# Kernel optimization log

Measured on AMD Instinct MI355X. Metric: run time of the kernel, lower is better.

The kernel has to match this reference:

```python
import jax, jax.numpy as jnp
import numpy as np

EPS = 1e-3  # keras LayerNormalization default epsilon

def layer_norm(x, gamma, beta):
    mu = jnp.mean(x, axis=-1, keepdims=True)
    var = jnp.var(x, axis=-1, keepdims=True)
    return (x - mu) * jax.lax.rsqrt(var + EPS) * gamma + beta

def setup_inputs() -> dict:
    key = jax.random.key(0)
    ks = jax.random.split(key, 10)
    B, N, FD, AD, PD, DP = 4, 512, 256, 256, 128, 64
    s = lambda k, *sh: jax.random.normal(k, sh, dtype=jnp.float32)
    return {
        "F": s(ks[0], B, N, FD),
        "D": s(ks[1], B, N, N, DP),
        "Wq": s(ks[2], FD, AD) / np.sqrt(FD),
        "Wk": s(ks[3], FD, AD) / np.sqrt(FD),
        "Wv": s(ks[4], FD, AD) / np.sqrt(FD),
        "g_f": jnp.ones((FD,), jnp.float32),
        "b_f": jnp.zeros((FD,), jnp.float32),
        "g_p": jnp.ones((DP,), jnp.float32),
        "b_p": jnp.zeros((DP,), jnp.float32),
        "W_pt": s(ks[5], DP, PD) / np.sqrt(DP),
        "b_pt": jnp.zeros((PD,), jnp.float32),
        "W_ph": s(ks[6], PD, 1) / np.sqrt(PD),
    }

def reference(F, D, Wq, Wk, Wv, g_f, b_f, g_p, b_p, W_pt, b_pt, W_ph):
    # features path
    Fn = layer_norm(F, g_f, b_f)                       # [B,N,FD]
    Q = Fn @ Wq                                        # [B,N,AD]
    K = Fn @ Wk
    V = Fn @ Wv
    # pair-bias path: LN -> Dense(pairs_dim)+bias -> Dense(num_heads=1)
    Bn = layer_norm(D, g_p, b_p)                       # [B,N,N,DP]
    Bt = Bn @ W_pt + b_pt                              # [B,N,N,PD]
    bias = (Bt @ W_ph)[..., 0]                         # [B,N,N]
    scalar = 1.0 / jnp.sqrt(jnp.float32(Q.shape[-1]))
    A = jnp.einsum('bqd,bkd->bqk', Q, K) + bias        # QK^T + pair bias
    A = jax.nn.softmax(scalar * A, axis=-1)
    O = jnp.einsum('bqk,bkd->bqd', A, V)               # [B,N,AD]
    return jnp.sum(O, axis=-1)                         # [B,N]
```

## Files before the change

### kernel.cpp

```cpp
#include <hip/hip_runtime.h>
#include <cstddef>
#include <cstdint>

#define OFF_GW    0
#define OFF_WV    64
#define OFF_SC    320
#define OFF_VSUM  384
#define OFF_Q     2432
#define OFF_K     526720

typedef float v4f __attribute__((ext_vector_type(4)));

__global__ __launch_bounds__(256) void k0_consts(
    const float* __restrict__ Wv, const float* __restrict__ g_p,
    const float* __restrict__ b_p, const float* __restrict__ W_pt,
    const float* __restrict__ b_pt, const float* __restrict__ W_ph,
    float* __restrict__ ws) {
  int t = threadIdx.x;
  if (blockIdx.x < 64) {
    int row = blockIdx.x * 4 + (t >> 6);
    int l = t & 63;
    float s = 0.f;
#pragma unroll
    for (int j = 0; j < 4; ++j) s += Wv[row * 256 + l + 64 * j];
    for (int m = 32; m >= 1; m >>= 1) s += __shfl_xor(s, m);
    if (l == 0) ws[OFF_WV + row] = s;
  } else {
    __shared__ float wc_s[64];
    __shared__ float wph_s[128];
    if (t < 128) wph_s[t] = W_ph[t];
    __syncthreads();
    int c = t >> 2, sub = t & 3;
    float wc = 0.f;
#pragma unroll
    for (int j = 0; j < 32; ++j)
      wc += W_pt[c * 128 + sub * 32 + j] * wph_s[sub * 32 + j];
    wc += __shfl_xor(wc, 1);
    wc += __shfl_xor(wc, 2);
    if (sub == 0) {
      wc_s[c] = wc;
      ws[OFF_GW + c] = g_p[c] * wc;
    }
    __syncthreads();
    if (t == 0) {
      float sg = 0.f, bc = 0.f;
      for (int cc = 0; cc < 64; ++cc) {
        sg += g_p[cc] * wc_s[cc];
        bc += b_p[cc] * wc_s[cc];
      }
      for (int p = 0; p < 128; ++p) bc += b_pt[p] * wph_s[p];
      ws[OFF_SC] = sg;
      ws[OFF_SC + 1] = bc;
    }
  }
}

__global__ __launch_bounds__(256) void k1_ln_qk(
    const float* __restrict__ F, const float* __restrict__ Wq,
    const float* __restrict__ Wk, const float* __restrict__ g_f,
    const float* __restrict__ b_f, float* __restrict__ ws) {
  __shared__ __align__(16) float fn[8][260];
  __shared__ float smu[8], srn[8];
  int t = threadIdx.x;
  int g = blockIdx.x >> 1, h = blockIdx.x & 1;
  int row0 = g * 8;
  const float* Fp = F + (size_t)row0 * 256;
#pragma unroll
  for (int k = 0; k < 8; ++k) fn[k][t] = Fp[k * 256 + t];
  __syncthreads();
  int r = t >> 5, l32 = t & 31;
  float s1 = 0.f, s2 = 0.f;
#pragma unroll
  for (int m = 0; m < 8; ++m) {
    float x = fn[r][l32 + 32 * m];
    s1 += x;
    s2 += x * x;
  }
  for (int m = 16; m >= 1; m >>= 1) {
    s1 += __shfl_xor(s1, m);
    s2 += __shfl_xor(s2, m);
  }
  if (l32 == 0) {
    float mu = s1 * (1.f / 256.f);
    float var = s2 * (1.f / 256.f) - mu * mu;
    smu[r] = mu;
    srn[r] = rsqrtf(var + 1e-3f);
  }
  __syncthreads();
  float gf = g_f[t], bf = b_f[t];
#pragma unroll
  for (int k = 0; k < 8; ++k)
    fn[k][t] = (fn[k][t] - smu[k]) * srn[k] * gf + bf;
  __syncthreads();
  if (h == 0) {
    const float* wv = ws + OFF_WV;
    float s = 0.f;
#pragma unroll
    for (int m = 0; m < 8; ++m) s += fn[r][l32 + 32 * m] * wv[l32 + 32 * m];
    for (int m = 16; m >= 1; m >>= 1) s += __shfl_xor(s, m);
    if (l32 == 0) ws[OFF_VSUM + row0 + r] = s;
  }
  int matsel = t >> 7;
  int col = h * 128 + (t & 127);
  const float* W = matsel ? Wk : Wq;
  float acc[8] = {0, 0, 0, 0, 0, 0, 0, 0};
#pragma unroll 2
  for (int f = 0; f < 256; f += 4) {
    float w0 = W[(f + 0) * 256 + col];
    float w1 = W[(f + 1) * 256 + col];
    float w2 = W[(f + 2) * 256 + col];
    float w3 = W[(f + 3) * 256 + col];
#pragma unroll
    for (int k = 0; k < 8; ++k) {
      v4f x = *(const v4f*)(&fn[k][f]);
      acc[k] = fmaf(x.w, w3,
               fmaf(x.z, w2, fmaf(x.y, w1, fmaf(x.x, w0, acc[k]))));
    }
  }
  float* Out = ws + (matsel ? OFF_K : OFF_Q) + (size_t)row0 * 256 + col;
#pragma unroll
  for (int k = 0; k < 8; ++k) Out[k * 256] = acc[k];
}

__global__ __launch_bounds__(256) void kb_bias_attn(
    const float* __restrict__ D, const float* __restrict__ ws,
    float* __restrict__ out) {
  __shared__ float Sx[4][512];
  __shared__ __align__(16) float Qs[4][256];
  __shared__ float vs[512];
  int t = threadIdx.x;
  int w = t >> 6, l = t & 63;
  int b = blockIdx.x >> 7, tile = blockIdx.x & 127;
  int rowbase = b * 512 + tile * 4;

#pragma unroll
  for (int k = 0; k < 4; ++k)
    Qs[k][t] = ws[OFF_Q + (size_t)(rowbase + k) * 256 + t];
  vs[t] = ws[OFF_VSUM + b * 512 + t];
  vs[t + 256] = ws[OFF_VSUM + b * 512 + 256 + t];
  float sum_gw = ws[OFF_SC];
  float bconst = ws[OFF_SC + 1];
  v4f g[16];
#pragma unroll
  for (int p = 0; p < 16; ++p) g[p] = *(const v4f*)(ws + OFF_GW + p * 4);

  const float* Dw = D + (size_t)(rowbase + w) * (512 * 64);
#pragma unroll 1
  for (int i = 0; i < 8; ++i) {
    const v4f* e = (const v4f*)(Dw + (size_t)(i * 64 + l) * 64);
    v4f x[16];
#pragma unroll
    for (int p = 0; p < 16; ++p) x[p] = e[p];
    float s1 = 0.f, s2 = 0.f, sw = 0.f;
#pragma unroll
    for (int p = 0; p < 16; ++p) {
      v4f xx = x[p];
      s1 += xx.x + xx.y + xx.z + xx.w;
      s2 += xx.x * xx.x + xx.y * xx.y + xx.z * xx.z + xx.w * xx.w;
      sw += xx.x * g[p].x + xx.y * g[p].y + xx.z * g[p].z + xx.w * g[p].w;
    }
    float mu = s1 * (1.f / 64.f);
    float var = s2 * (1.f / 64.f) - mu * mu;
    float rn = rsqrtf(var + 1e-3f);
    Sx[w][i * 64 + l] = (rn * (sw - mu * sum_gw) + bconst) * 0.0625f;
  }
  __syncthreads();

  const float* Kg = ws + OFF_K;
  const v4f* K0p = (const v4f*)(Kg + (size_t)(b * 512 + t) * 256);
  const v4f* K1p = (const v4f*)(Kg + (size_t)(b * 512 + 256 + t) * 256);
  float a0[4] = {0, 0, 0, 0}, a1[4] = {0, 0, 0, 0};
#pragma unroll 8
  for (int f = 0; f < 64; ++f) {
    v4f kv0 = K0p[f];
    v4f kv1 = K1p[f];
#pragma unroll
    for (int rr = 0; rr < 4; ++rr) {
      v4f qv = *(const v4f*)(&Qs[rr][f * 4]);
      a0[rr] += qv.x * kv0.x + qv.y * kv0.y + qv.z * kv0.z + qv.w * kv0.w;
      a1[rr] += qv.x * kv1.x + qv.y * kv1.y + qv.z * kv1.z + qv.w * kv1.w;
    }
  }
#pragma unroll
  for (int rr = 0; rr < 4; ++rr) {
    Sx[rr][t] += a0[rr] * 0.0625f;
    Sx[rr][t + 256] += a1[rr] * 0.0625f;
  }
  __syncthreads();

  float m = -1e30f;
#pragma unroll
  for (int j = 0; j < 8; ++j) m = fmaxf(m, Sx[w][l + 64 * j]);
  for (int mm = 32; mm >= 1; mm >>= 1) m = fmaxf(m, __shfl_xor(m, mm));
  float se = 0.f, sv = 0.f;
#pragma unroll
  for (int j = 0; j < 8; ++j) {
    float ev = __expf(Sx[w][l + 64 * j] - m);
    se += ev;
    sv += ev * vs[l + 64 * j];
  }
  for (int mm = 32; mm >= 1; mm >>= 1) {
    se += __shfl_xor(se, mm);
    sv += __shfl_xor(sv, mm);
  }
  if (l == 0) out[rowbase + w] = sv / se;
}

extern "C" void kernel_launch(void* const* d_in, const int* in_sizes, int n_in,
                              void* d_out, int out_size, void* d_ws,
                              size_t ws_size, hipStream_t stream) {
  const float* F    = (const float*)d_in[0];
  const float* D    = (const float*)d_in[1];
  const float* Wq   = (const float*)d_in[2];
  const float* Wk   = (const float*)d_in[3];
  const float* Wv   = (const float*)d_in[4];
  const float* g_f  = (const float*)d_in[5];
  const float* b_f  = (const float*)d_in[6];
  const float* g_p  = (const float*)d_in[7];
  const float* b_p  = (const float*)d_in[8];
  const float* W_pt = (const float*)d_in[9];
  const float* b_pt = (const float*)d_in[10];
  const float* W_ph = (const float*)d_in[11];
  float* out = (float*)d_out;
  float* ws = (float*)d_ws;

  k0_consts<<<65, 256, 0, stream>>>(Wv, g_p, b_p, W_pt, b_pt, W_ph, ws);
  k1_ln_qk<<<512, 256, 0, stream>>>(F, Wq, Wk, g_f, b_f, ws);
  kb_bias_attn<<<512, 256, 0, stream>>>(D, ws, out);
}
```

Before: 443.1 us.

## Transpose K in workspace and coalesce D loads with 16-lane row reductions

K is now written transposed per batch, [col][row], so the attention kernel reads contiguous float2 pairs across threads instead of strided rows of K. Reading D changes from one thread per 64-float row to 16 lanes cooperating on each row with v4f loads, followed by shuffle reductions. Both changes target uncoalesced global memory access in the bandwidth-bound pair-bias stage. In exchange there are many more shuffle instructions, and the transposed K stores in k1 are scattered writes.

```diff
diff --git a/kernel.cpp b/kernel.cpp
--- a/kernel.cpp
+++ b/kernel.cpp
@@ -7,9 +7,10 @@
 #define OFF_SC    320
 #define OFF_VSUM  384
 #define OFF_Q     2432
-#define OFF_K     526720
+#define OFF_KT    526720
 
 typedef float v4f __attribute__((ext_vector_type(4)));
+typedef float v2f __attribute__((ext_vector_type(2)));
 
 __global__ __launch_bounds__(256) void k0_consts(
     const float* __restrict__ Wv, const float* __restrict__ g_p,
@@ -117,9 +118,18 @@
                fmaf(x.z, w2, fmaf(x.y, w1, fmaf(x.x, w0, acc[k]))));
     }
   }
-  float* Out = ws + (matsel ? OFF_K : OFF_Q) + (size_t)row0 * 256 + col;
-#pragma unroll
-  for (int k = 0; k < 8; ++k) Out[k * 256] = acc[k];
+  if (matsel == 0) {
+    float* Out = ws + OFF_Q + (size_t)row0 * 256 + col;
+#pragma unroll
+    for (int k = 0; k < 8; ++k) Out[k * 256] = acc[k];
+  } else {
+    int bb = row0 >> 9, r0b = row0 & 511;
+    float* Out = ws + OFF_KT + (size_t)bb * 131072 + (size_t)col * 512 + r0b;
+    v4f o0 = {acc[0], acc[1], acc[2], acc[3]};
+    v4f o1 = {acc[4], acc[5], acc[6], acc[7]};
+    *(v4f*)Out = o0;
+    *(v4f*)(Out + 4) = o1;
+  }
 }
 
 __global__ __launch_bounds__(256) void kb_bias_attn(
@@ -140,51 +150,52 @@
   vs[t + 256] = ws[OFF_VSUM + b * 512 + 256 + t];
   float sum_gw = ws[OFF_SC];
   float bconst = ws[OFF_SC + 1];
-  v4f g[16];
-#pragma unroll
-  for (int p = 0; p < 16; ++p) g[p] = *(const v4f*)(ws + OFF_GW + p * 4);
-
+
+  int l16 = l & 15, lg = l >> 4;
+  v4f gv = *(const v4f*)(ws + OFF_GW + l16 * 4);
   const float* Dw = D + (size_t)(rowbase + w) * (512 * 64);
-#pragma unroll 1
-  for (int i = 0; i < 8; ++i) {
-    const v4f* e = (const v4f*)(Dw + (size_t)(i * 64 + l) * 64);
-    v4f x[16];
-#pragma unroll
-    for (int p = 0; p < 16; ++p) x[p] = e[p];
-    float s1 = 0.f, s2 = 0.f, sw = 0.f;
-#pragma unroll
-    for (int p = 0; p < 16; ++p) {
-      v4f xx = x[p];
-      s1 += xx.x + xx.y + xx.z + xx.w;
-      s2 += xx.x * xx.x + xx.y * xx.y + xx.z * xx.z + xx.w * xx.w;
-      sw += xx.x * g[p].x + xx.y * g[p].y + xx.z * g[p].z + xx.w * g[p].w;
-    }
-    float mu = s1 * (1.f / 64.f);
-    float var = s2 * (1.f / 64.f) - mu * mu;
-    float rn = rsqrtf(var + 1e-3f);
-    Sx[w][i * 64 + l] = (rn * (sw - mu * sum_gw) + bconst) * 0.0625f;
-  }
-  __syncthreads();
-
-  const float* Kg = ws + OFF_K;
-  const v4f* K0p = (const v4f*)(Kg + (size_t)(b * 512 + t) * 256);
-  const v4f* K1p = (const v4f*)(Kg + (size_t)(b * 512 + 256 + t) * 256);
+#pragma unroll 8
+  for (int i = 0; i < 128; ++i) {
+    v4f x = *(const v4f*)(Dw + (size_t)(4 * i + lg) * 64 + l16 * 4);
+    float s1 = x.x + x.y + x.z + x.w;
+    float s2 = x.x * x.x + x.y * x.y + x.z * x.z + x.w * x.w;
+    float sw = x.x * gv.x + x.y * gv.y + x.z * gv.z + x.w * gv.w;
+#pragma unroll
+    for (int m = 1; m <= 8; m <<= 1) {
+      s1 += __shfl_xor(s1, m);
+      s2 += __shfl_xor(s2, m);
+      sw += __shfl_xor(sw, m);
+    }
+    if (l16 == 0) {
+      float mu = s1 * (1.f / 64.f);
+      float var = s2 * (1.f / 64.f) - mu * mu;
+      float rn = rsqrtf(var + 1e-3f);
+      Sx[w][4 * i + lg] = (rn * (sw - mu * sum_gw) + bconst) * 0.0625f;
+    }
+  }
+  __syncthreads();
+
+  const float* Ktb = ws + OFF_KT + (size_t)b * 131072;
   float a0[4] = {0, 0, 0, 0}, a1[4] = {0, 0, 0, 0};
-#pragma unroll 8
-  for (int f = 0; f < 64; ++f) {
-    v4f kv0 = K0p[f];
-    v4f kv1 = K1p[f];
-#pragma unroll
-    for (int rr = 0; rr < 4; ++rr) {
-      v4f qv = *(const v4f*)(&Qs[rr][f * 4]);
-      a0[rr] += qv.x * kv0.x + qv.y * kv0.y + qv.z * kv0.z + qv.w * kv0.w;
-      a1[rr] += qv.x * kv1.x + qv.y * kv1.y + qv.z * kv1.z + qv.w * kv1.w;
+#pragma unroll 2
+  for (int f4 = 0; f4 < 64; ++f4) {
+    v4f qv0 = *(const v4f*)(&Qs[0][f4 * 4]);
+    v4f qv1 = *(const v4f*)(&Qs[1][f4 * 4]);
+    v4f qv2 = *(const v4f*)(&Qs[2][f4 * 4]);
+    v4f qv3 = *(const v4f*)(&Qs[3][f4 * 4]);
+#pragma unroll
+    for (int ff = 0; ff < 4; ++ff) {
+      v2f kv = *(const v2f*)(Ktb + (size_t)(f4 * 4 + ff) * 512 + 2 * t);
+      a0[0] += qv0[ff] * kv.x; a1[0] += qv0[ff] * kv.y;
+      a0[1] += qv1[ff] * kv.x; a1[1] += qv1[ff] * kv.y;
+      a0[2] += qv2[ff] * kv.x; a1[2] += qv2[ff] * kv.y;
+      a0[3] += qv3[ff] * kv.x; a1[3] += qv3[ff] * kv.y;
     }
   }
 #pragma unroll
   for (int rr = 0; rr < 4; ++rr) {
-    Sx[rr][t] += a0[rr] * 0.0625f;
-    Sx[rr][t + 256] += a1[rr] * 0.0625f;
+    Sx[rr][2 * t]     += a0[rr] * 0.0625f;
+    Sx[rr][2 * t + 1] += a1[rr] * 0.0625f;
   }
   __syncthreads();
 
```

After: 454.8 us. +2.7%, slower.

## Split bias-attention into 2-row blocks of 512 threads for more parallelism

Applied to the files above, without the earlier changes.

Restructures the main bias-attention kernel so each 512-thread block handles two query rows instead of four. Eight waves share the per-pair LayerNorm work on D, and the gamma*w vector moves from registers into shared memory. This launches more blocks and waves to hide memory latency while streaming D. In exchange, each K tile is reused by fewer query rows, so K is read from cache twice as often, and half the waves idle during the softmax.

```diff
diff --git a/kernel.cpp b/kernel.cpp
--- a/kernel.cpp
+++ b/kernel.cpp
@@ -122,88 +122,85 @@
   for (int k = 0; k < 8; ++k) Out[k * 256] = acc[k];
 }
 
-__global__ __launch_bounds__(256) void kb_bias_attn(
+__global__ __launch_bounds__(512, 4) void kb_bias_attn(
     const float* __restrict__ D, const float* __restrict__ ws,
     float* __restrict__ out) {
-  __shared__ float Sx[4][512];
-  __shared__ __align__(16) float Qs[4][256];
+  __shared__ float Sx[2][512];
+  __shared__ __align__(16) float Qs[2][256];
   __shared__ float vs[512];
+  __shared__ __align__(16) float gws[64];
   int t = threadIdx.x;
   int w = t >> 6, l = t & 63;
-  int b = blockIdx.x >> 7, tile = blockIdx.x & 127;
-  int rowbase = b * 512 + tile * 4;
-
-#pragma unroll
-  for (int k = 0; k < 4; ++k)
-    Qs[k][t] = ws[OFF_Q + (size_t)(rowbase + k) * 256 + t];
+  int b = blockIdx.x >> 8, pair = blockIdx.x & 255;
+  int rowbase = b * 512 + pair * 2;
+
+  if (t < 256) Qs[0][t] = ws[OFF_Q + (size_t)rowbase * 256 + t];
+  else         Qs[1][t - 256] = ws[OFF_Q + (size_t)(rowbase + 1) * 256 + (t - 256)];
   vs[t] = ws[OFF_VSUM + b * 512 + t];
-  vs[t + 256] = ws[OFF_VSUM + b * 512 + 256 + t];
+  if (t < 64) gws[t] = ws[OFF_GW + t];
   float sum_gw = ws[OFF_SC];
   float bconst = ws[OFF_SC + 1];
-  v4f g[16];
-#pragma unroll
-  for (int p = 0; p < 16; ++p) g[p] = *(const v4f*)(ws + OFF_GW + p * 4);
-
-  const float* Dw = D + (size_t)(rowbase + w) * (512 * 64);
+  __syncthreads();
+
+  {
+    int row = w >> 2, quar = w & 3;
+    const float* Dw = D + (size_t)(rowbase + row) * (512 * 64);
 #pragma unroll 1
-  for (int i = 0; i < 8; ++i) {
-    const v4f* e = (const v4f*)(Dw + (size_t)(i * 64 + l) * 64);
-    v4f x[16];
-#pragma unroll
-    for (int p = 0; p < 16; ++p) x[p] = e[p];
-    float s1 = 0.f, s2 = 0.f, sw = 0.f;
-#pragma unroll
-    for (int p = 0; p < 16; ++p) {
-      v4f xx = x[p];
-      s1 += xx.x + xx.y + xx.z + xx.w;
-      s2 += xx.x * xx.x + xx.y * xx.y + xx.z * xx.z + xx.w * xx.w;
-      sw += xx.x * g[p].x + xx.y * g[p].y + xx.z * g[p].z + xx.w * g[p].w;
-    }
-    float mu = s1 * (1.f / 64.f);
-    float var = s2 * (1.f / 64.f) - mu * mu;
-    float rn = rsqrtf(var + 1e-3f);
-    Sx[w][i * 64 + l] = (rn * (sw - mu * sum_gw) + bconst) * 0.0625f;
-  }
-  __syncthreads();
-
-  const float* Kg = ws + OFF_K;
-  const v4f* K0p = (const v4f*)(Kg + (size_t)(b * 512 + t) * 256);
-  const v4f* K1p = (const v4f*)(Kg + (size_t)(b * 512 + 256 + t) * 256);
-  float a0[4] = {0, 0, 0, 0}, a1[4] = {0, 0, 0, 0};
+    for (int i = 0; i < 2; ++i) {
+      int e = quar * 128 + i * 64 + l;
+      const v4f* ep = (const v4f*)(Dw + (size_t)e * 64);
+      v4f x[16];
+#pragma unroll
+      for (int p = 0; p < 16; ++p) x[p] = ep[p];
+      float s1 = 0.f, s2 = 0.f, sw = 0.f;
+#pragma unroll
+      for (int p = 0; p < 16; ++p) {
+        v4f xx = x[p];
+        v4f gv = *(const v4f*)(&gws[p * 4]);
+        s1 += xx.x + xx.y + xx.z + xx.w;
+        s2 += xx.x * xx.x + xx.y * xx.y + xx.z * xx.z + xx.w * xx.w;
+        sw += xx.x * gv.x + xx.y * gv.y + xx.z * gv.z + xx.w * gv.w;
+      }
+      float mu = s1 * (1.f / 64.f);
+      float var = s2 * (1.f / 64.f) - mu * mu;
+      float rn = rsqrtf(var + 1e-3f);
+      Sx[row][e] = (rn * (sw - mu * sum_gw) + bconst) * 0.0625f;
+    }
+  }
+  __syncthreads();
+
+  const float* Kp = ws + OFF_K + (size_t)(b * 512 + t) * 256;
+  float a0 = 0.f, a1 = 0.f;
 #pragma unroll 8
-  for (int f = 0; f < 64; ++f) {
-    v4f kv0 = K0p[f];
-    v4f kv1 = K1p[f];
-#pragma unroll
-    for (int rr = 0; rr < 4; ++rr) {
-      v4f qv = *(const v4f*)(&Qs[rr][f * 4]);
-      a0[rr] += qv.x * kv0.x + qv.y * kv0.y + qv.z * kv0.z + qv.w * kv0.w;
-      a1[rr] += qv.x * kv1.x + qv.y * kv1.y + qv.z * kv1.z + qv.w * kv1.w;
-    }
-  }
-#pragma unroll
-  for (int rr = 0; rr < 4; ++rr) {
-    Sx[rr][t] += a0[rr] * 0.0625f;
-    Sx[rr][t + 256] += a1[rr] * 0.0625f;
-  }
-  __syncthreads();
-
-  float m = -1e30f;
-#pragma unroll
-  for (int j = 0; j < 8; ++j) m = fmaxf(m, Sx[w][l + 64 * j]);
-  for (int mm = 32; mm >= 1; mm >>= 1) m = fmaxf(m, __shfl_xor(m, mm));
-  float se = 0.f, sv = 0.f;
-#pragma unroll
-  for (int j = 0; j < 8; ++j) {
-    float ev = __expf(Sx[w][l + 64 * j] - m);
-    se += ev;
-    sv += ev * vs[l + 64 * j];
-  }
-  for (int mm = 32; mm >= 1; mm >>= 1) {
-    se += __shfl_xor(se, mm);
-    sv += __shfl_xor(sv, mm);
-  }
-  if (l == 0) out[rowbase + w] = sv / se;
+  for (int f4 = 0; f4 < 64; ++f4) {
+    v4f kv = ((const v4f*)Kp)[f4];
+    v4f q0 = *(const v4f*)(&Qs[0][f4 * 4]);
+    v4f q1 = *(const v4f*)(&Qs[1][f4 * 4]);
+    a0 += q0.x * kv.x + q0.y * kv.y + q0.z * kv.z + q0.w * kv.w;
+    a1 += q1.x * kv.x + q1.y * kv.y + q1.z * kv.z + q1.w * kv.w;
+  }
+  Sx[0][t] += a0 * 0.0625f;
+  Sx[1][t] += a1 * 0.0625f;
+  __syncthreads();
+
+  if (w < 2) {
+    float m = -1e30f;
+#pragma unroll
+    for (int j = 0; j < 8; ++j) m = fmaxf(m, Sx[w][l + 64 * j]);
+    for (int mm = 32; mm >= 1; mm >>= 1) m = fmaxf(m, __shfl_xor(m, mm));
+    float se = 0.f, sv = 0.f;
+#pragma unroll
+    for (int j = 0; j < 8; ++j) {
+      float ev = __expf(Sx[w][l + 64 * j] - m);
+      se += ev;
+      sv += ev * vs[l + 64 * j];
+    }
+    for (int mm = 32; mm >= 1; mm >>= 1) {
+      se += __shfl_xor(se, mm);
+      sv += __shfl_xor(sv, mm);
+    }
+    if (l == 0) out[rowbase + w] = sv / se;
+  }
 }
 
 extern "C" void kernel_launch(void* const* d_in, const int* in_sizes, int n_in,
@@ -226,5 +223,5 @@
 
   k0_consts<<<65, 256, 0, stream>>>(Wv, g_p, b_p, W_pt, b_pt, W_ph, ws);
   k1_ln_qk<<<512, 256, 0, stream>>>(F, Wq, Wk, g_f, b_f, ws);
-  kb_bias_attn<<<512, 256, 0, stream>>>(D, ws, out);
-}
+  kb_bias_attn<<<1024, 512, 0, stream>>>(D, ws, out);
+}
```

New measurement: 475.7 us. 7.4% more time.
